# Kernel tuning notes

Hardware: AMD Instinct MI355X
Metric: run time of the kernel (lower is better)

## Reference

```python
import jax, jax.numpy as jnp
import numpy as np
import math

EMBED = 1024
HEADS = 16
HEAD_DIM = EMBED // HEADS  # 64
BSZ = 32
TGT = 512   # == src_len, required by the bmm-over-sequence structure
SRC = 512   # == BSZ*HEADS, required by the need_weights view


def _xavier(k, shape):
    fan_out, fan_in = shape
    limit = math.sqrt(6.0 / (fan_in + fan_out))
    return jax.random.uniform(k, shape, jnp.float32, -limit, limit)


def setup_inputs() -> dict:
    key = jax.random.key(0)
    ks = jax.random.split(key, 8)
    d = EMBED
    return {
        # query given as [bsz, tgt_len, d]; the module transposes it internally
        "query": jax.random.normal(ks[0], (BSZ, TGT, d), jnp.float32),
        "key": jax.random.normal(ks[1], (SRC, BSZ, d), jnp.float32),
        "value": jax.random.normal(ks[2], (SRC, BSZ, d), jnp.float32),
        "Wq": _xavier(ks[3], (d, d)), "bq": jnp.zeros((d,), jnp.float32),
        "Wk": _xavier(ks[4], (d, d)), "bk": jnp.zeros((d,), jnp.float32),
        "Wv": _xavier(ks[5], (d, d)), "bv": jnp.zeros((d,), jnp.float32),
        "Wo": _xavier(ks[6], (d, d)), "bo": jnp.zeros((d,), jnp.float32),
    }


def reference(query, key, value, Wq, bq, Wk, bk, Wv, bv, Wo, bo):
    H, hd = HEADS, HEAD_DIM
    # module transposes [bsz, tgt_len, d] -> [tgt_len, bsz, d]
    query = jnp.transpose(query, (1, 0, 2))
    T, B, D = query.shape
    S = key.shape[0]  # == T and == B*H by construction
    # projections (nn.Linear: x @ W.T + b)
    q = (query @ Wq.T + bq).reshape(T, B * H, hd)
    k = (key @ Wk.T + bk).reshape(S, B * H, hd)
    v = (value @ Wv.T + bv).reshape(S, B * H, hd)
    # torch.bmm with the SEQUENCE dim as the bmm batch dim (faithful to source):
    # scores: [T, BH, BH]
    scores = jnp.einsum('tbd,tcd->tbc', q, k) / jnp.sqrt(jnp.asarray(hd, q.dtype))
    attn = jax.nn.softmax(scores, axis=-1)  # dropout p=0.0, eval mode
    out = jnp.einsum('tbc,tcd->tbd', attn, v)  # [T, BH, hd]
    out = out.reshape(T, B, D) @ Wo.T + bo     # [T, B, D]
    # need_weights=True branch: view [T,H,B,S], permute(2,1,0,3), mean over heads
    w = attn.reshape(T, H, B, S).transpose(2, 1, 0, 3).mean(axis=1)  # [B, T, S]
    return out, w
```

## Files before the change

### kernel.cpp

```cpp
#include <hip/hip_runtime.h>
#include <hip/hip_bf16.h>
#include <stdint.h>


typedef __attribute__((ext_vector_type(8))) short bf16x8;
typedef __attribute__((ext_vector_type(4))) float f32x4;
typedef unsigned short u16;
typedef unsigned int u32;

typedef __attribute__((address_space(1))) const unsigned int as1_u32;
typedef __attribute__((address_space(3))) unsigned int as3_u32;

__device__ __forceinline__ void glds16(const void* g, void* l) {
    __builtin_amdgcn_global_load_lds((as1_u32*)g, (as3_u32*)l, 16, 0, 0);
}

__device__ __forceinline__ u16 f2bf(float f) {
    u32 u = __builtin_bit_cast(u32, f);
    u32 r = (u + 0x7FFFu + ((u >> 16) & 1u)) >> 16;
    return (u16)r;
}

__device__ __forceinline__ u32 cvtpk(float a, float b) {
    u32 r;
    asm("v_cvt_pk_bf16_f32 %0, %1, %2" : "=v"(r) : "v"(a), "v"(b));
    return r;
}

template <int CTRL>
__device__ __forceinline__ float dpp_add(float x) {
    int xi = __builtin_bit_cast(int, x);
    int yi = __builtin_amdgcn_update_dpp(0, xi, CTRL, 0xF, 0xF, true);
    return x + __builtin_bit_cast(float, yi);
}
__device__ __forceinline__ float red16(float v) {
    v = dpp_add<0xB1>(v);
    v = dpp_add<0x4E>(v);
    v = dpp_add<0x141>(v);
    v = dpp_add<0x140>(v);
    return v;
}

__global__ void convw_kernel(const float4* __restrict__ query,
                             const float4* __restrict__ key,
                             const float4* __restrict__ value,
                             const float4* __restrict__ Wq, const float4* __restrict__ Wk,
                             const float4* __restrict__ Wv, const float4* __restrict__ Wo,
                             uint2* __restrict__ qx, uint2* __restrict__ kx,
                             uint2* __restrict__ vx,
                             uint2* __restrict__ wqb, uint2* __restrict__ wkb,
                             uint2* __restrict__ wvb, uint2* __restrict__ wob) {
    const int NT = gridDim.x * blockDim.x;
    for (int i = blockIdx.x * blockDim.x + threadIdx.x; i < 13631488; i += NT) {
        float4 v; uint2* d; int di;
        if (i < 4194304) {
            int m = i >> 8, c4 = i & 255;
            int t = m >> 5, b = m & 31;
            v = query[(b * 512 + t) * 256 + c4];
            d = qx; di = i;
        } else if (i < 8388608) {
            di = i - 4194304; v = key[di]; d = kx;
        } else if (i < 12582912) {
            di = i - 8388608; v = value[di]; d = vx;
        } else {
            int jj = i - 12582912;
            int wsel = jj >> 18; di = jj & 262143;
            const float4* s = wsel == 0 ? Wq : wsel == 1 ? Wk : wsel == 2 ? Wv : Wo;
            d = wsel == 0 ? wqb : wsel == 1 ? wkb : wsel == 2 ? wvb : wob;
            v = s[di];
        }
        uint2 r;
        r.x = (u32)f2bf(v.x) | ((u32)f2bf(v.y) << 16);
        r.y = (u32)f2bf(v.z) | ((u32)f2bf(v.w) << 16);
        d[di] = r;
    }
}

template <int F32OUT>
__global__ __launch_bounds__(256, 2)
void gemm_bb(const u16* __restrict__ A0, const u16* __restrict__ A1,
             const u16* __restrict__ A2,
             const u16* __restrict__ B0, const u16* __restrict__ B1,
             const u16* __restrict__ B2,
             const float* __restrict__ b0, const float* __restrict__ b1,
             const float* __restrict__ b2,
             void* __restrict__ C0, void* __restrict__ C1, void* __restrict__ C2) {
    __shared__ __align__(16) u16 As[8192];
    __shared__ __align__(16) u16 Bs[8192];
    const int z = blockIdx.z;
    const u16* A = z == 0 ? A0 : z == 1 ? A1 : A2;
    const u16* B = z == 0 ? B0 : z == 1 ? B1 : B2;
    const float* bias = z == 0 ? b0 : z == 1 ? b1 : b2;
    void* Cp = z == 0 ? C0 : z == 1 ? C1 : C2;
    const int tid = threadIdx.x;
    const int id = blockIdx.x;
    const int xcd = id & 7, j = id >> 3;
    const int ny = j & 7, band = xcd * 16 + (j >> 3);
    const long N0 = (long)ny * 128;
    const long M0 = (long)band * 128;
    const int lane = tid & 63, wv = tid >> 6;
    const int l15 = lane & 15, g = lane >> 4;
    const int wm = (wv >> 1) * 64, wn = (wv & 1) * 64;

    auto gldsAB = [&](int kt) {
#pragma unroll
        for (int i2 = 0; i2 < 4; ++i2) {
            int q = tid + 256 * i2; int r = q >> 3, c16 = q & 7;
            int c16s = c16 ^ (r & 7);
            char* lbA = (char*)As + (i2 * 256 + wv * 64) * 16;
            char* lbB = (char*)Bs + (i2 * 256 + wv * 64) * 16;
            glds16(A + (M0 + r) * 1024 + kt * 64 + c16s * 8, lbA);
            glds16(B + (N0 + r) * 1024 + kt * 64 + c16s * 8, lbB);
        }
    };
    f32x4 acc[4][4] = {};
    const int swz = (l15 & 7) << 4;
    for (int kt = 0; kt < 16; ++kt) {
        gldsAB(kt);
        __syncthreads();
#pragma unroll
        for (int kk = 0; kk < 2; ++kk) {
            bf16x8 av[4], bvv[4];
#pragma unroll
            for (int mt = 0; mt < 4; ++mt) {
                int row = wm + mt * 16 + l15;
                av[mt] = *(const bf16x8*)((const char*)As + row * 128 + ((kk * 64 + g * 16) ^ swz));
            }
#pragma unroll
            for (int nt = 0; nt < 4; ++nt) {
                int row = wn + nt * 16 + l15;
                bvv[nt] = *(const bf16x8*)((const char*)Bs + row * 128 + ((kk * 64 + g * 16) ^ swz));
            }
#pragma unroll
            for (int mt = 0; mt < 4; ++mt)
#pragma unroll
                for (int nt = 0; nt < 4; ++nt)
                    acc[mt][nt] = __builtin_amdgcn_mfma_f32_16x16x32_bf16(av[mt], bvv[nt], acc[mt][nt], 0, 0, 0);
        }
        __syncthreads();
    }
    float bsv[4];
#pragma unroll
    for (int nt = 0; nt < 4; ++nt) bsv[nt] = bias[N0 + wn + nt * 16 + l15];
#pragma unroll
    for (int mt = 0; mt < 4; ++mt)
#pragma unroll
        for (int nt = 0; nt < 4; ++nt)
#pragma unroll
            for (int r = 0; r < 4; ++r) {
                long m = M0 + wm + mt * 16 + g * 4 + r;
                long n = N0 + wn + nt * 16 + l15;
                float v = acc[mt][nt][r] + bsv[nt];
                if (F32OUT) ((float*)Cp)[m * 1024 + n] = v;
                else        ((u16*)Cp)[m * 1024 + n] = f2bf(v);
            }
}

__global__ __launch_bounds__(256)
void vtrans_kernel(const u16* __restrict__ v_ws, u16* __restrict__ vt) {
    __shared__ __align__(16) u16 tl[64][136];
    const int bid = blockIdx.x;
    const int t = bid >> 2, c0 = (bid & 3) * 128;
    const u16* src = v_ws + (size_t)t * 32768 + (size_t)c0 * 64;
#pragma unroll
    for (int i = 0; i < 4; ++i) {
        int ch = i * 256 + threadIdx.x;
        int rc = ch >> 3, e0 = (ch & 7) * 8;
        bf16x8 v8 = *(const bf16x8*)(src + rc * 64 + e0);
#pragma unroll
        for (int j = 0; j < 8; ++j) tl[e0 + j][rc] = (u16)v8[j];
    }
    __syncthreads();
    u16* dst = vt + (size_t)t * 32768 + c0;
#pragma unroll
    for (int i = 0; i < 4; ++i) {
        int ch = i * 256 + threadIdx.x;
        int e = ch >> 4, cc = (ch & 15) * 8;
        *(bf16x8*)(dst + (size_t)e * 512 + cc) = *(const bf16x8*)(&tl[e][cc]);
    }
}

__global__ __launch_bounds__(512, 2)
void attn_kernel(const u16* __restrict__ Q, const u16* __restrict__ K,
                 const u16* __restrict__ VT, u16* __restrict__ ctx,
                 float* __restrict__ wout) {
    __shared__ __align__(16) char smem[65536];
    const int bid = blockIdx.x;
    const int wk_ = (bid & 7) * 256 + (bid >> 3);
    const int t = wk_ >> 2, it = wk_ & 3;
    const int tid = threadIdx.x, lane = tid & 63, wv = tid >> 6;
    const int l15 = lane & 15, g = lane >> 4;
    const int swk = (l15 & 7) << 4;
    const int bb = it * 8 + wv;
    const float ksc = 0.18033688011112042f;

    const u16* Kt = K + (size_t)t * 32768;
    const u16* Vtt = VT + (size_t)t * 32768;

    {
#pragma unroll
        for (int hh = 0; hh < 8; ++hh) {
            int idx = hh * 512 + tid;
            int sl = idx >> 3, c16 = idx & 7;
            int csw = c16 ^ (sl & 7);
            glds16(Kt + (size_t)sl * 64 + csw * 8, smem + hh * 8192 + wv * 1024);
        }
    }
    const int c = 32 * l15 + bb;
    const u16* qrow = Q + ((size_t)t * 512 + c) * 64;
    bf16x8 qb0 = *(const bf16x8*)(qrow + g * 8);
    bf16x8 qb1 = *(const bf16x8*)(qrow + 32 + g * 8);
    __syncthreads();

    float sum = 0.f;
    bf16x8 pP[16];
    __builtin_amdgcn_s_setprio(1);
#pragma unroll
    for (int mq = 0; mq < 16; ++mq) {
        union { bf16x8 v; u32 u[4]; } pa;
#pragma unroll
        for (int h2 = 0; h2 < 2; ++h2) {
            int lsl = 2 * mq + h2;
            const char* rowp = smem + (lsl * 16 + l15) * 128;
            bf16x8 a0 = *(const bf16x8*)(rowp + ((g * 16) ^ swk));
            bf16x8 a1 = *(const bf16x8*)(rowp + ((64 + g * 16) ^ swk));
            f32x4 zz = {0.f, 0.f, 0.f, 0.f};
            zz = __builtin_amdgcn_mfma_f32_16x16x32_bf16(a0, qb0, zz, 0, 0, 0);
            zz = __builtin_amdgcn_mfma_f32_16x16x32_bf16(a1, qb1, zz, 0, 0, 0);
            float e0 = exp2f(zz[0] * ksc), e1 = exp2f(zz[1] * ksc);
            float e2 = exp2f(zz[2] * ksc), e3 = exp2f(zz[3] * ksc);
            sum += (e0 + e1) + (e2 + e3);
            pa.u[2 * h2]     = cvtpk(e0, e1);
            pa.u[2 * h2 + 1] = cvtpk(e2, e3);
        }
        pP[mq] = pa.v;
    }
    __builtin_amdgcn_s_setprio(0);
    sum += __shfl_xor(sum, 16);
    sum += __shfl_xor(sum, 32);
    const float inv = 1.f / sum;
    __syncthreads();

    {
#pragma unroll
        for (int hh = 0; hh < 8; ++hh) {
            int ch = hh * 512 + tid;
            int e = ch >> 6, c6 = ch & 63;
            int csw = c6 ^ (e & 7);
            glds16(Vtt + (size_t)e * 512 + csw * 8, smem + hh * 8192 + wv * 1024);
        }
    }
    {
        const float inv16 = inv * 0.0625f;
        float4 wreg0 = {0.f, 0.f, 0.f, 0.f}, wreg1 = {0.f, 0.f, 0.f, 0.f};
#pragma unroll
        for (int st = 0; st < 32; ++st) {
            union { bf16x8 v; u32 u[4]; } pu; pu.v = pP[st >> 1];
            u32 ua = pu.u[(st & 1) * 2], ub = pu.u[(st & 1) * 2 + 1];
            float v0 = __builtin_bit_cast(float, (ua & 0xFFFFu) << 16) * inv16;
            float v1 = __builtin_bit_cast(float, ua & 0xFFFF0000u) * inv16;
            float v2 = __builtin_bit_cast(float, (ub & 0xFFFFu) << 16) * inv16;
            float v3 = __builtin_bit_cast(float, ub & 0xFFFF0000u) * inv16;
            v0 = red16(v0); v1 = red16(v1); v2 = red16(v2); v3 = red16(v3);
            if ((st >> 1) == l15) {
                if (st & 1) wreg1 = (float4){v0, v1, v2, v3};
                else        wreg0 = (float4){v0, v1, v2, v3};
            }
        }
        float* wrow = wout + ((size_t)(bb * 512 + t)) * 512 + 32 * l15 + 4 * g;
        *(float4*)(wrow) = wreg0;
        *(float4*)(wrow + 16) = wreg1;
    }
    __syncthreads();

    f32x4 pv[4];
#pragma unroll
    for (int nt = 0; nt < 4; ++nt) pv[nt] = (f32x4){0.f, 0.f, 0.f, 0.f};
    __builtin_amdgcn_s_setprio(1);
#pragma unroll
    for (int mq = 0; mq < 16; ++mq) {
        bf16x8 pa = pP[mq];
#pragma unroll
        for (int nt = 0; nt < 4; ++nt) {
            int e = nt * 16 + l15;
            const char* vrow = smem + e * 1024;
            int off = mq * 64 + 8 * g;
            union { bf16x8 v; uint2 uu[2]; } bv;
            bv.uu[0] = *(const uint2*)(vrow + (off ^ swk));
            bv.uu[1] = *(const uint2*)(vrow + ((off + 32) ^ swk));
            pv[nt] = __builtin_amdgcn_mfma_f32_16x16x32_bf16(pa, bv.v, pv[nt], 0, 0, 0);
        }
    }
    __builtin_amdgcn_s_setprio(0);

    float invv[4];
#pragma unroll
    for (int r = 0; r < 4; ++r) invv[r] = __shfl(inv, g * 4 + r);
#pragma unroll
    for (int nt = 0; nt < 4; ++nt)
#pragma unroll
        for (int r = 0; r < 4; ++r)
            ctx[((size_t)t * 512 + 32 * (g * 4 + r) + bb) * 64 + nt * 16 + l15] =
                f2bf(pv[nt][r] * invv[r]);
}

extern "C" void kernel_launch(void* const* d_in, const int* in_sizes, int n_in,
                              void* d_out, int out_size, void* d_ws, size_t ws_size,
                              hipStream_t stream) {
    const float* query = (const float*)d_in[0];
    const float* key   = (const float*)d_in[1];
    const float* value = (const float*)d_in[2];
    const float* Wq = (const float*)d_in[3];  const float* bq = (const float*)d_in[4];
    const float* Wk = (const float*)d_in[5];  const float* bk = (const float*)d_in[6];
    const float* Wv = (const float*)d_in[7];  const float* bv = (const float*)d_in[8];
    const float* Wo = (const float*)d_in[9];  const float* bo = (const float*)d_in[10];

    char* ws = (char*)d_ws;
    u16* wqb  = (u16*)(ws + 0);
    u16* wkb  = (u16*)(ws + 2097152);
    u16* wvb  = (u16*)(ws + 4194304);
    u16* wob  = (u16*)(ws + 6291456);
    u16* q_ws = (u16*)(ws + 8388608);
    u16* k_ws = (u16*)(ws + 41943040);
    u16* v_ws = (u16*)(ws + 75497472);
    u16* qx   = (u16*)(ws + 109051904);

    float* out  = (float*)d_out;
    float* wout = out + 16777216;
    u16* kx = (u16*)d_out;
    u16* vx = (u16*)((char*)d_out + 33554432);
    u16* vt = (u16*)((char*)d_out + 33554432);

    convw_kernel<<<2048, 256, 0, stream>>>(
        (const float4*)query, (const float4*)key, (const float4*)value,
        (const float4*)Wq, (const float4*)Wk, (const float4*)Wv, (const float4*)Wo,
        (uint2*)qx, (uint2*)kx, (uint2*)vx,
        (uint2*)wqb, (uint2*)wkb, (uint2*)wvb, (uint2*)wob);

    dim3 gg3(1024, 1, 3);
    gemm_bb<0><<<gg3, 256, 0, stream>>>(qx, kx, vx, wqb, wkb, wvb,
                                        bq, bk, bv, q_ws, k_ws, v_ws);

    vtrans_kernel<<<2048, 256, 0, stream>>>(v_ws, vt);

    attn_kernel<<<2048, 512, 0, stream>>>(q_ws, k_ws, vt, q_ws, wout);

    gemm_bb<1><<<dim3(1024, 1, 1), 256, 0, stream>>>(q_ws, q_ws, q_ws,
                                                     wob, wob, wob, bo, bo, bo,
                                                     out, out, out);
}
```

Baseline: 325.1 us.

## Fold softmax scale into Wq, swap DPP reductions for shuffles, raise GEMM occupancy

Pre-multiplies Wq (and bq through a new per-projection scale argument) by the log2e/sqrt(d) factor during the bf16 conversion. This removes the per-score multiply inside the attention kernel. It also replaces the DPP row-reduction with __shfl_xor butterflies, simplifies the bf16 unpack masks, and raises the GEMM launch bounds to 3 waves per SIMD. Scaling before rounding to bf16 slightly changes numerics, the shuffle reduction may be slower than DPP, and the tighter register budget may cause spills.

```diff
diff --git a/kernel.cpp b/kernel.cpp
--- a/kernel.cpp
+++ b/kernel.cpp
@@ -11,6 +11,8 @@
 typedef __attribute__((address_space(1))) const unsigned int as1_u32;
 typedef __attribute__((address_space(3))) unsigned int as3_u32;
 
+#define KSC 0.18033688011112042f
+
 __device__ __forceinline__ void glds16(const void* g, void* l) {
     __builtin_amdgcn_global_load_lds((as1_u32*)g, (as3_u32*)l, 16, 0, 0);
 }
@@ -27,17 +29,11 @@
     return r;
 }
 
-template <int CTRL>
-__device__ __forceinline__ float dpp_add(float x) {
-    int xi = __builtin_bit_cast(int, x);
-    int yi = __builtin_amdgcn_update_dpp(0, xi, CTRL, 0xF, 0xF, true);
-    return x + __builtin_bit_cast(float, yi);
-}
-__device__ __forceinline__ float red16(float v) {
-    v = dpp_add<0xB1>(v);
-    v = dpp_add<0x4E>(v);
-    v = dpp_add<0x141>(v);
-    v = dpp_add<0x140>(v);
+__device__ __forceinline__ float red16s(float v) {
+    v += __shfl_xor(v, 1);
+    v += __shfl_xor(v, 2);
+    v += __shfl_xor(v, 4);
+    v += __shfl_xor(v, 8);
     return v;
 }
 
@@ -68,6 +64,7 @@
             const float4* s = wsel == 0 ? Wq : wsel == 1 ? Wk : wsel == 2 ? Wv : Wo;
             d = wsel == 0 ? wqb : wsel == 1 ? wkb : wsel == 2 ? wvb : wob;
             v = s[di];
+            if (wsel == 0) { v.x *= KSC; v.y *= KSC; v.z *= KSC; v.w *= KSC; }
         }
         uint2 r;
         r.x = (u32)f2bf(v.x) | ((u32)f2bf(v.y) << 16);
@@ -77,13 +74,14 @@
 }
 
 template <int F32OUT>
-__global__ __launch_bounds__(256, 2)
+__global__ __launch_bounds__(256, 3)
 void gemm_bb(const u16* __restrict__ A0, const u16* __restrict__ A1,
              const u16* __restrict__ A2,
              const u16* __restrict__ B0, const u16* __restrict__ B1,
              const u16* __restrict__ B2,
              const float* __restrict__ b0, const float* __restrict__ b1,
              const float* __restrict__ b2,
+             float s0, float s1, float s2,
              void* __restrict__ C0, void* __restrict__ C1, void* __restrict__ C2) {
     __shared__ __align__(16) u16 As[8192];
     __shared__ __align__(16) u16 Bs[8192];
@@ -91,6 +89,7 @@
     const u16* A = z == 0 ? A0 : z == 1 ? A1 : A2;
     const u16* B = z == 0 ? B0 : z == 1 ? B1 : B2;
     const float* bias = z == 0 ? b0 : z == 1 ? b1 : b2;
+    const float bsc = z == 0 ? s0 : z == 1 ? s1 : s2;
     void* Cp = z == 0 ? C0 : z == 1 ? C1 : C2;
     const int tid = threadIdx.x;
     const int id = blockIdx.x;
@@ -141,7 +140,7 @@
     }
     float bsv[4];
 #pragma unroll
-    for (int nt = 0; nt < 4; ++nt) bsv[nt] = bias[N0 + wn + nt * 16 + l15];
+    for (int nt = 0; nt < 4; ++nt) bsv[nt] = bias[N0 + wn + nt * 16 + l15] * bsc;
 #pragma unroll
     for (int mt = 0; mt < 4; ++mt)
 #pragma unroll
@@ -192,7 +191,6 @@
     const int l15 = lane & 15, g = lane >> 4;
     const int swk = (l15 & 7) << 4;
     const int bb = it * 8 + wv;
-    const float ksc = 0.18033688011112042f;
 
     const u16* Kt = K + (size_t)t * 32768;
     const u16* Vtt = VT + (size_t)t * 32768;
@@ -227,8 +225,8 @@
             f32x4 zz = {0.f, 0.f, 0.f, 0.f};
             zz = __builtin_amdgcn_mfma_f32_16x16x32_bf16(a0, qb0, zz, 0, 0, 0);
             zz = __builtin_amdgcn_mfma_f32_16x16x32_bf16(a1, qb1, zz, 0, 0, 0);
-            float e0 = exp2f(zz[0] * ksc), e1 = exp2f(zz[1] * ksc);
-            float e2 = exp2f(zz[2] * ksc), e3 = exp2f(zz[3] * ksc);
+            float e0 = exp2f(zz[0]), e1 = exp2f(zz[1]);
+            float e2 = exp2f(zz[2]), e3 = exp2f(zz[3]);
             sum += (e0 + e1) + (e2 + e3);
             pa.u[2 * h2]     = cvtpk(e0, e1);
             pa.u[2 * h2 + 1] = cvtpk(e2, e3);
@@ -257,11 +255,11 @@
         for (int st = 0; st < 32; ++st) {
             union { bf16x8 v; u32 u[4]; } pu; pu.v = pP[st >> 1];
             u32 ua = pu.u[(st & 1) * 2], ub = pu.u[(st & 1) * 2 + 1];
-            float v0 = __builtin_bit_cast(float, (ua & 0xFFFFu) << 16) * inv16;
+            float v0 = __builtin_bit_cast(float, ua << 16) * inv16;
             float v1 = __builtin_bit_cast(float, ua & 0xFFFF0000u) * inv16;
-            float v2 = __builtin_bit_cast(float, (ub & 0xFFFFu) << 16) * inv16;
+            float v2 = __builtin_bit_cast(float, ub << 16) * inv16;
             float v3 = __builtin_bit_cast(float, ub & 0xFFFF0000u) * inv16;
-            v0 = red16(v0); v1 = red16(v1); v2 = red16(v2); v3 = red16(v3);
+            v0 = red16s(v0); v1 = red16s(v1); v2 = red16s(v2); v3 = red16s(v3);
             if ((st >> 1) == l15) {
                 if (st & 1) wreg1 = (float4){v0, v1, v2, v3};
                 else        wreg0 = (float4){v0, v1, v2, v3};
@@ -339,7 +337,8 @@
 
     dim3 gg3(1024, 1, 3);
     gemm_bb<0><<<gg3, 256, 0, stream>>>(qx, kx, vx, wqb, wkb, wvb,
-                                        bq, bk, bv, q_ws, k_ws, v_ws);
+                                        bq, bk, bv, KSC, 1.f, 1.f,
+                                        q_ws, k_ws, v_ws);
 
     vtrans_kernel<<<2048, 256, 0, stream>>>(v_ws, vt);
 
@@ -347,5 +346,6 @@
 
     gemm_bb<1><<<dim3(1024, 1, 1), 256, 0, stream>>>(q_ws, q_ws, q_ws,
                                                      wob, wob, wob, bo, bo, bo,
+                                                     1.f, 1.f, 1.f,
                                                      out, out, out);
 }
```

New measurement: 381.4 us. +17.3%, slower.
